# Kernel tuning notes

Hardware: AMD Instinct MI355X
Metric: run time of the kernel (lower is better)

Reference implementation:

```python
import jax, jax.numpy as jnp
import numpy as np

# Conv hyperparams (from init_kwargs)
STRIDE = (1, 1)
PADDING = (1, 1)
DILATION = (1, 1)

AQMIN, AQMAX = 0.0, 15.0   # uint4 activation range
WQMIN, WQMAX = -8.0, 7.0   # int4 weight range


def setup_inputs() -> dict:
    key = jax.random.key(0)
    k1, k2 = jax.random.split(key)
    # Activations in [0, 16) so uint4 quantization is non-trivial
    x = jax.random.uniform(k1, (32, 64, 112, 112), dtype=jnp.float32) * 16.0
    # Weights spread over int4 range
    w = jax.random.normal(k2, (128, 64, 3, 3), dtype=jnp.float32) * 4.0
    return {"x": x, "w": w}


def reference(x, w):
    # Quantize: activations -> uint4 [0,15], weights -> int4 [-8,7]
    q_in = jnp.clip(jnp.round(x), AQMIN, AQMAX)
    q_w = jnp.clip(jnp.round(w), WQMIN, WQMAX)
    # im2col unfold + matmul in the original == standard convolution.
    # Integer-valued fp32 math is exact here (|acc| << 2^24).
    out = jax.lax.conv_general_dilated(
        q_in, q_w,
        window_strides=STRIDE,
        padding=[(PADDING[0], PADDING[0]), (PADDING[1], PADDING[1])],
        rhs_dilation=DILATION,
        dimension_numbers=("NCHW", "OIHW", "NCHW"),
    )
    return out.astype(jnp.float32)  # [32, 128, 112, 112]
```

## Files before the change

kernel.cpp:

```cpp
#include <hip/hip_runtime.h>


#define CIN  64
#define HH   112
#define WW   112
#define HW   (HH * WW)
#define COUT 128
#define KTOT 576
#define HP   114
#define WP   114
#define LDSW 592

#define XQ_BYTES (32 * HP * WP * 64)
#define NWBLK 288
#define NXBLK (32 * 57)
#define NCONV 1568

typedef __attribute__((ext_vector_type(4))) int int32x4;

__global__ __launch_bounds__(256) void k_prep(const float* __restrict__ x,
                                              const float* __restrict__ w,
                                              char* __restrict__ xq,
                                              char* __restrict__ wq) {
    const int bid = blockIdx.x, tid = threadIdx.x;
    if (bid < NWBLK) {
        int idx = bid * 256 + tid;
        int o  = idx / KTOT;
        int r  = idx % KTOT;
        int kh = r / 192;
        int kw = (r / 64) % 3;
        int c  = r % 64;
        float q = fminf(fmaxf(rintf(w[((o * CIN + c) * 3 + kh) * 3 + kw]), -8.0f), 7.0f);
        wq[idx] = (char)(int)q;
        return;
    }
    const int rid = bid - NWBLK;
    const int n  = rid / 57;
    const int hp = (rid % 57) * 2 + (tid >> 7);
    const int wp = tid & 127;
    if (wp >= WP) return;
    char* dst = xq + (((size_t)n * HP + hp) * WP + wp) * 64;
    int32x4* d4 = (int32x4*)dst;
    if (hp == 0 || hp == HP - 1 || wp == 0 || wp == WP - 1) {
#pragma unroll
        for (int i = 0; i < 4; ++i) d4[i] = (int32x4)(0);
        return;
    }
    const int h = hp - 1, ww = wp - 1;
    const float* px = x + (((size_t)n * CIN) * HH + h) * WW + ww;
    unsigned int buf[16];
#pragma unroll
    for (int cw = 0; cw < 16; ++cw) {
        unsigned int word = 0;
#pragma unroll
        for (int j = 0; j < 4; ++j) {
            float v = px[(size_t)(cw * 4 + j) * HW];
            float q = fminf(fmaxf(rintf(v), 0.0f), 15.0f);
            word |= ((unsigned int)(int)q) << (8 * j);
        }
        buf[cw] = word;
    }
#pragma unroll
    for (int i = 0; i < 4; ++i) {
        int32x4 v;
        v.x = (int)buf[i * 4 + 0];
        v.y = (int)buf[i * 4 + 1];
        v.z = (int)buf[i * 4 + 2];
        v.w = (int)buf[i * 4 + 3];
        d4[i] = v;
    }
}

__global__ __launch_bounds__(256) void k_conv(const char* __restrict__ xq,
                                              const char* __restrict__ wq,
                                              float* __restrict__ out) {
    __shared__ char wlds[64 * LDSW];

    const int tid = threadIdx.x;
    const int nid  = (blockIdx.x & 7) * (NCONV / 8) + (blockIdx.x >> 3);
    const int half = nid & 1;
    const int pb   = nid >> 1;

    const char* wsrc = wq + (size_t)half * (64 * KTOT);
    for (int i = tid; i < 64 * (KTOT / 16); i += 256) {
        int row = i / 36, ch = i % 36;
        *(int32x4*)(&wlds[row * LDSW + ch * 16]) =
            *(const int32x4*)(wsrc + row * KTOT + ch * 16);
    }
    __syncthreads();

    const int wave = tid >> 6;
    const int lane = tid & 63;
    const int l15  = lane & 15;
    const int lk   = lane >> 4;
    const int cobase = 0;

#pragma unroll
    for (int it = 0; it < 2; ++it) {
        const int chunk = pb * 2 + it;
        const int n  = chunk / 49;
        const int s0 = (chunk % 49) * 256 + wave * 64;
        const char* xbase = xq + (size_t)n * (HP * WP * 64);

        int saddr[4];
#pragma unroll
        for (int tS = 0; tS < 4; ++tS) {
            int sl = s0 + tS * 16 + l15;
            int hh = sl / WW;
            int ww = sl - hh * WW;
            saddr[tS] = (hh * WP + ww) * 64 + lk * 16;
        }

        int32x4 acc[4][4];
#pragma unroll
        for (int i = 0; i < 4; ++i)
#pragma unroll
            for (int j = 0; j < 4; ++j) acc[i][j] = (int32x4)(0);

        int32x4 af[4], afn[4];
#pragma unroll
        for (int tS = 0; tS < 4; ++tS)
            af[tS] = *(const int32x4*)(xbase + saddr[tS]);

#pragma unroll
        for (int ks = 0; ks < 9; ++ks) {
            if (ks < 8) {
                const int ksn = ks + 1;
                const int koffn = ((ksn / 3) * WP + (ksn % 3)) * 64;
#pragma unroll
                for (int tS = 0; tS < 4; ++tS)
                    afn[tS] = *(const int32x4*)(xbase + saddr[tS] + koffn);
            }
#pragma unroll
            for (int tO = 0; tO < 4; ++tO) {
                const int32x4 bf = *(const int32x4*)(
                    &wlds[(cobase + tO * 16 + l15) * LDSW + lk * 16 + ks * 64]);
#pragma unroll
                for (int tS = 0; tS < 4; ++tS)
                    acc[tS][tO] = __builtin_amdgcn_mfma_i32_16x16x64_i8(af[tS], bf, acc[tS][tO], 0, 0, 0);
            }
#pragma unroll
            for (int tS = 0; tS < 4; ++tS) af[tS] = afn[tS];
        }

        float* obase = out + (size_t)n * (COUT * HW) + (size_t)half * 64 * HW;
#pragma unroll
        for (int tS = 0; tS < 4; ++tS) {
#pragma unroll
            for (int tO = 0; tO < 4; ++tO) {
                const int co = tO * 16 + l15;
                const int sl = s0 + tS * 16 + lk * 4;
                float4 v;
                v.x = (float)acc[tS][tO][0];
                v.y = (float)acc[tS][tO][1];
                v.z = (float)acc[tS][tO][2];
                v.w = (float)acc[tS][tO][3];
                *(float4*)(&obase[(size_t)co * HW + sl]) = v;
            }
        }
    }
}

extern "C" void kernel_launch(void* const* d_in, const int* in_sizes, int n_in,
                              void* d_out, int out_size, void* d_ws, size_t ws_size,
                              hipStream_t stream) {
    const float* x = (const float*)d_in[0];
    const float* w = (const float*)d_in[1];
    float* out = (float*)d_out;

    char* xq = (char*)d_ws;
    char* wq = xq + XQ_BYTES;

    hipLaunchKernelGGL(k_prep, dim3(NWBLK + NXBLK), dim3(256), 0, stream, x, w, xq, wq);
    hipLaunchKernelGGL(k_conv, dim3(NCONV), dim3(256), 0, stream, xq, wq, out);
}
```

Baseline: 105.9 us.

## Share activation tiles across both output-channel halves and coalesce prep stores via LDS

The conv kernel now uses 512-thread blocks with all 128 output channels' weights in LDS. Waves are paired so both channel halves read the same spatial tile, instead of separate blocks each loading the activations for their half. The prep kernel stages packed uint4 activations in shared memory and writes them out as contiguous 16-byte chunks, replacing scattered per-thread 64-byte stores. The cost is doubled LDS per block (about 74KB) and larger blocks, which may lower occupancy.

```diff
diff --git a/kernel.cpp b/kernel.cpp
--- a/kernel.cpp
+++ b/kernel.cpp
@@ -22,6 +22,7 @@
                                               const float* __restrict__ w,
                                               char* __restrict__ xq,
                                               char* __restrict__ wq) {
+    __shared__ char xsl[4 * 4096];
     const int bid = blockIdx.x, tid = threadIdx.x;
     if (bid < NWBLK) {
         int idx = bid * 256 + tid;
@@ -35,57 +36,54 @@
         return;
     }
     const int rid = bid - NWBLK;
-    const int n  = rid / 57;
-    const int hp = (rid % 57) * 2 + (tid >> 7);
-    const int wp = tid & 127;
-    if (wp >= WP) return;
-    char* dst = xq + (((size_t)n * HP + hp) * WP + wp) * 64;
-    int32x4* d4 = (int32x4*)dst;
-    if (hp == 0 || hp == HP - 1 || wp == 0 || wp == WP - 1) {
-#pragma unroll
-        for (int i = 0; i < 4; ++i) d4[i] = (int32x4)(0);
-        return;
-    }
-    const int h = hp - 1, ww = wp - 1;
-    const float* px = x + (((size_t)n * CIN) * HH + h) * WW + ww;
-    unsigned int buf[16];
+    const int n   = rid / 57;
+    const int hp0 = (rid % 57) * 2;
+    const int hp  = hp0 + (tid >> 7);
+    const int wp  = tid & 127;
+    const bool inb = (hp >= 1) && (hp <= HH) && (wp >= 1) && (wp <= WW);
+    const float* px = x + (((size_t)n * CIN) * HH + (hp - 1)) * WW + (wp - 1);
 #pragma unroll
     for (int cw = 0; cw < 16; ++cw) {
         unsigned int word = 0;
+        if (inb) {
 #pragma unroll
-        for (int j = 0; j < 4; ++j) {
-            float v = px[(size_t)(cw * 4 + j) * HW];
-            float q = fminf(fmaxf(rintf(v), 0.0f), 15.0f);
-            word |= ((unsigned int)(int)q) << (8 * j);
+            for (int j = 0; j < 4; ++j) {
+                float v = px[(size_t)(cw * 4 + j) * HW];
+                float q = fminf(fmaxf(rintf(v), 0.0f), 15.0f);
+                word |= ((unsigned int)(int)q) << (8 * j);
+            }
         }
-        buf[cw] = word;
+        *(unsigned int*)(&xsl[(cw >> 2) * 4096 + tid * 16 + (cw & 3) * 4]) = word;
     }
+    __syncthreads();
 #pragma unroll
-    for (int i = 0; i < 4; ++i) {
-        int32x4 v;
-        v.x = (int)buf[i * 4 + 0];
-        v.y = (int)buf[i * 4 + 1];
-        v.z = (int)buf[i * 4 + 2];
-        v.w = (int)buf[i * 4 + 3];
-        d4[i] = v;
+    for (int k = 0; k < 4; ++k) {
+        const int u   = tid + k * 256;
+        const int r   = u >> 9;
+        const int rem = u & 511;
+        const int dwp = rem >> 2;
+        const int ch  = rem & 3;
+        if (dwp < WP) {
+            int32x4 v = *(const int32x4*)(&xsl[ch * 4096 + (r * 128 + dwp) * 16]);
+            *(int32x4*)(xq + (((size_t)n * HP + hp0 + r) * WP + dwp) * 64 + ch * 16) = v;
+        }
     }
 }
 
-__global__ __launch_bounds__(256) void k_conv(const char* __restrict__ xq,
+__global__ __launch_bounds__(512) void k_conv(const char* __restrict__ xq,
                                               const char* __restrict__ wq,
                                               float* __restrict__ out) {
-    __shared__ char wlds[64 * LDSW];
+    __shared__ char wlds[COUT * LDSW];
 
     const int tid = threadIdx.x;
-    const int nid  = (blockIdx.x & 7) * (NCONV / 8) + (blockIdx.x >> 3);
-    const int half = nid & 1;
-    const int pb   = nid >> 1;
+    const int nid   = (blockIdx.x & 7) * (NCONV / 8) + (blockIdx.x >> 3);
+    const int n     = nid / 49;
+    const int chunk = nid % 49;
 
-    const char* wsrc = wq + (size_t)half * (64 * KTOT);
-    for (int i = tid; i < 64 * (KTOT / 16); i += 256) {
+    for (int i = tid; i < COUT * (KTOT / 16); i += 512) {
         int row = i / 36, ch = i % 36;
         *(int32x4*)(&wlds[row * LDSW + ch * 16]) =
-            *(const int32x4*)(wsrc + row * KTOT + ch * 16);
+            *(const int32x4*)(wq + row * KTOT + ch * 16);
     }
     __syncthreads();
 
@@ -93,70 +91,66 @@
     const int lane = tid & 63;
     const int l15  = lane & 15;
     const int lk   = lane >> 4;
-    const int cobase = 0;
+    const int spg  = wave >> 1;
+    const int cobase = (wave & 1) * 64;
+
+    const int s0 = chunk * 256 + spg * 64;
+    const char* xbase = xq + (size_t)n * (HP * WP * 64);
+
+    int saddr[4];
+#pragma unroll
+    for (int tS = 0; tS < 4; ++tS) {
+        int sl = s0 + tS * 16 + l15;
+        int hh = sl / WW;
+        int ww = sl - hh * WW;
+        saddr[tS] = (hh * WP + ww) * 64 + lk * 16;
+    }
+
+    int32x4 acc[4][4];
+#pragma unroll
+    for (int i = 0; i < 4; ++i)
+#pragma unroll
+        for (int j = 0; j < 4; ++j) acc[i][j] = (int32x4)(0);
+
+    int32x4 af[4], afn[4];
+#pragma unroll
+    for (int tS = 0; tS < 4; ++tS)
+        af[tS] = *(const int32x4*)(xbase + saddr[tS]);
 
 #pragma unroll
-    for (int it = 0; it < 2; ++it) {
-        const int chunk = pb * 2 + it;
-        const int n  = chunk / 49;
-        const int s0 = (chunk % 49) * 256 + wave * 64;
-        const char* xbase = xq + (size_t)n * (HP * WP * 64);
+    for (int ks = 0; ks < 9; ++ks) {
+        if (ks < 8) {
+            const int ksn = ks + 1;
+            const int koffn = ((ksn / 3) * WP + (ksn % 3)) * 64;
+#pragma unroll
+            for (int tS = 0; tS < 4; ++tS)
+                afn[tS] = *(const int32x4*)(xbase + saddr[tS] + koffn);
+        }
+#pragma unroll
+        for (int tO = 0; tO < 4; ++tO) {
+            const int32x4 bf = *(const int32x4*)(
+                &wlds[(cobase + tO * 16 + l15) * LDSW + lk * 16 + ks * 64]);
+#pragma unroll
+            for (int tS = 0; tS < 4; ++tS)
+                acc[tS][tO] = __builtin_amdgcn_mfma_i32_16x16x64_i8(af[tS], bf, acc[tS][tO], 0, 0, 0);
+        }
+#pragma unroll
+        for (int tS = 0; tS < 4; ++tS) af[tS] = afn[tS];
+    }
 
-        int saddr[4];
+    float* obase = out + (size_t)n * (COUT * HW);
 #pragma unroll
-        for (int tS = 0; tS < 4; ++tS) {
-            int sl = s0 + tS * 16 + l15;
-            int hh = sl / WW;
-            int ww = sl - hh * WW;
-            saddr[tS] = (hh * WP + ww) * 64 + lk * 16;
-        }
-
-        int32x4 acc[4][4];
+    for (int tS = 0; tS < 4; ++tS) {
 #pragma unroll
-        for (int i = 0; i < 4; ++i)
-#pragma unroll
-            for (int j = 0; j < 4; ++j) acc[i][j] = (int32x4)(0);
-
-        int32x4 af[4], afn[4];
-#pragma unroll
-        for (int tS = 0; tS < 4; ++tS)
-            af[tS] = *(const int32x4*)(xbase + saddr[tS]);
-
-#pragma unroll
-        for (int ks = 0; ks < 9; ++ks) {
-            if (ks < 8) {
-                const int ksn = ks + 1;
-                const int koffn = ((ksn / 3) * WP + (ksn % 3)) * 64;
-#pragma unroll
-                for (int tS = 0; tS < 4; ++tS)
-                    afn[tS] = *(const int32x4*)(xbase + saddr[tS] + koffn);
-            }
-#pragma unroll
-            for (int tO = 0; tO < 4; ++tO) {
-                const int32x4 bf = *(const int32x4*)(
-                    &wlds[(cobase + tO * 16 + l15) * LDSW + lk * 16 + ks * 64]);
-#pragma unroll
-                for (int tS = 0; tS < 4; ++tS)
-                    acc[tS][tO] = __builtin_amdgcn_mfma_i32_16x16x64_i8(af[tS], bf, acc[tS][tO], 0, 0, 0);
-            }
-#pragma unroll
-            for (int tS = 0; tS < 4; ++tS) af[tS] = afn[tS];
-        }
-
-        float* obase = out + (size_t)n * (COUT * HW) + (size_t)half * 64 * HW;
-#pragma unroll
-        for (int tS = 0; tS < 4; ++tS) {
-#pragma unroll
-            for (int tO = 0; tO < 4; ++tO) {
-                const int co = tO * 16 + l15;
-                const int sl = s0 + tS * 16 + lk * 4;
-                float4 v;
-                v.x = (float)acc[tS][tO][0];
-                v.y = (float)acc[tS][tO][1];
-                v.z = (float)acc[tS][tO][2];
-                v.w = (float)acc[tS][tO][3];
-                *(float4*)(&obase[(size_t)co * HW + sl]) = v;
-            }
+        for (int tO = 0; tO < 4; ++tO) {
+            const int co = cobase + tO * 16 + l15;
+            const int sl = s0 + tS * 16 + lk * 4;
+            float4 v;
+            v.x = (float)acc[tS][tO][0];
+            v.y = (float)acc[tS][tO][1];
+            v.z = (float)acc[tS][tO][2];
+            v.w = (float)acc[tS][tO][3];
+            *(float4*)(&obase[(size_t)co * HW + sl]) = v;
         }
     }
 }
@@ -172,5 +166,5 @@
     char* wq = xq + XQ_BYTES;
 
     hipLaunchKernelGGL(k_prep, dim3(NWBLK + NXBLK), dim3(256), 0, stream, x, w, xq, wq);
-    hipLaunchKernelGGL(k_conv, dim3(NCONV), dim3(256), 0, stream, xq, wq, out);
+    hipLaunchKernelGGL(k_conv, dim3(NCONV), dim3(512), 0, stream, xq, wq, out);
 }
```

Result: slower. 110.0 us (+4.0%).
